# Optimization experiments

Hardware: AMD Instinct MI355X
Metric: run time of the kernel (lower is better)

Reference implementation:

```python
import jax, jax.numpy as jnp
import numpy as np
import math

B, T, D = 2, 2048, 1024
H = 16
DH = D // H  # 64
ROPE_BASE = 10000.0


def _rope_tables(seq_len, d_head, dtype=jnp.float32):
    inv_freq = 1.0 / (ROPE_BASE ** (jnp.arange(0, d_head, 2, dtype=jnp.float32) / d_head))
    pos = jnp.arange(seq_len, dtype=jnp.float32)
    freqs = jnp.outer(pos, inv_freq)            # [T, DH/2]
    emb = jnp.concatenate([freqs, freqs], -1)   # [T, DH]
    return jnp.cos(emb).astype(dtype), jnp.sin(emb).astype(dtype)


def _rotate_half(x):
    half = x.shape[-1] // 2
    return jnp.concatenate([-x[..., half:], x[..., :half]], axis=-1)


def setup_inputs() -> dict:
    key = jax.random.key(0)
    k1, k2, k3 = jax.random.split(key, 3)
    x = jax.random.normal(k1, (B, T, D), dtype=jnp.float32)
    qkv_w = jax.random.normal(k2, (D, 3 * D), dtype=jnp.float32) * (1.0 / math.sqrt(D))
    out_w = jax.random.normal(k3, (D, D), dtype=jnp.float32) * (1.0 / math.sqrt(D))
    out_b = jnp.zeros((D,), dtype=jnp.float32)
    mask = jnp.tril(jnp.ones((T, T), dtype=bool))[None, None]  # causal [1,1,T,T]
    return {"x": x, "mask": mask, "qkv_w": qkv_w, "out_w": out_w, "out_b": out_b}


def reference(x, mask, qkv_w, out_w, out_b):
    Bv, Tv, Dv = x.shape
    qkv = (x @ qkv_w).reshape(Bv, Tv, 3, H, DH)
    # [B, H, T, DH]
    q = jnp.transpose(qkv[:, :, 0], (0, 2, 1, 3))
    k = jnp.transpose(qkv[:, :, 1], (0, 2, 1, 3))
    v = jnp.transpose(qkv[:, :, 2], (0, 2, 1, 3))
    cos, sin = _rope_tables(Tv, DH, x.dtype)
    cos = cos[None, None]  # [1,1,T,DH]
    sin = sin[None, None]
    q = q * cos + _rotate_half(q) * sin
    k = k * cos + _rotate_half(k) * sin
    scores = jnp.einsum('bhqd,bhkd->bhqk', q, k) / math.sqrt(DH)
    scores = jnp.where(mask, scores, -jnp.inf)
    probs = jax.nn.softmax(scores, axis=-1)  # dropout = identity in eval mode
    out = jnp.einsum('bhqk,bhkd->bhqd', probs, v)
    out = jnp.transpose(out, (0, 2, 1, 3)).reshape(Bv, Tv, Dv)
    return out @ out_w + out_b
```

## Files before the change

### kernel.cpp

```cpp
#include <hip/hip_runtime.h>
#include <math.h>

typedef __attribute__((ext_vector_type(8))) short short8;
typedef __attribute__((ext_vector_type(4))) float f32x4;

static __device__ __forceinline__ unsigned short f2bf(float f) {
  unsigned u = __builtin_bit_cast(unsigned, f);
  u += 0x7fffu + ((u >> 16) & 1u);
  return (unsigned short)(u >> 16);
}
static __device__ __forceinline__ float bf2f(unsigned short h) {
  return __builtin_bit_cast(float, ((unsigned)h) << 16);
}
static __device__ __forceinline__ unsigned pack2bf(float a, float b) {
  return (unsigned)f2bf(a) | ((unsigned)f2bf(b) << 16);
}
static __device__ __forceinline__ unsigned pack2bf_t(float a, float b) {
  return __builtin_amdgcn_perm(__builtin_bit_cast(unsigned, b),
                               __builtin_bit_cast(unsigned, a), 0x07060302u);
}

typedef __attribute__((address_space(3))) unsigned short lds_us;
typedef __attribute__((address_space(1))) const unsigned short gbl_us;

static __device__ __forceinline__ void gld_lds16(const unsigned short* g,
                                                 unsigned short* l) {
  __builtin_amdgcn_global_load_lds((gbl_us*)g, (lds_us*)l, 16, 0, 0);
}

__global__ __launch_bounds__(256) void prep(const float* __restrict__ x,
                                            unsigned short* __restrict__ xb,
                                            const float* __restrict__ qkv_w,
                                            unsigned short* __restrict__ wqkvT,
                                            const float* __restrict__ out_w,
                                            unsigned short* __restrict__ woT) {
  __shared__ unsigned short T[64][68];
  const int blk = blockIdx.x;
  if (blk < 2048) {
    int i = (blk * 256 + threadIdx.x) * 8;
    float4 a = *(const float4*)(x + i);
    float4 b = *(const float4*)(x + i + 4);
    ushort4 u0 = {f2bf(a.x), f2bf(a.y), f2bf(a.z), f2bf(a.w)};
    ushort4 u1 = {f2bf(b.x), f2bf(b.y), f2bf(b.z), f2bf(b.w)};
    *(ushort4*)(xb + i) = u0;
    *(ushort4*)(xb + i + 4) = u1;
    return;
  }
  const float* in;
  unsigned short* out;
  int R, C, bx, by;
  if (blk < 2816) {
    in = qkv_w; out = wqkvT; R = 1024; C = 3072;
    bx = (blk - 2048) % 48; by = (blk - 2048) / 48;
  } else {
    in = out_w; out = woT; R = 1024; C = 1024;
    bx = (blk - 2816) % 16; by = (blk - 2816) / 16;
  }
  const int r0 = by * 64, c0 = bx * 64;
  const int tr = threadIdx.x >> 2;
  const int tc = (threadIdx.x & 3) * 16;
#pragma unroll
  for (int j = 0; j < 4; ++j) {
    float4 v = *(const float4*)(in + (size_t)(r0 + tr) * C + c0 + tc + j * 4);
    ushort4 u = {f2bf(v.x), f2bf(v.y), f2bf(v.z), f2bf(v.w)};
    *(ushort4*)&T[tr][tc + j * 4] = u;
  }
  __syncthreads();
  const int oc = tr;
#pragma unroll
  for (int g = 0; g < 4; ++g) {
    ushort4 u;
    u.x = T[tc + g * 4 + 0][oc];
    u.y = T[tc + g * 4 + 1][oc];
    u.z = T[tc + g * 4 + 2][oc];
    u.w = T[tc + g * 4 + 3][oc];
    *(ushort4*)(out + (size_t)(c0 + oc) * R + r0 + tc + g * 4) = u;
  }
}

template <int MODE, int TN>
__global__ __launch_bounds__(256) void gemm_mfma(
    const unsigned short* __restrict__ A, const unsigned short* __restrict__ BT,
    unsigned short* __restrict__ qo, unsigned short* __restrict__ ko,
    unsigned short* __restrict__ vo, const float* __restrict__ bias,
    float* __restrict__ out) {
  constexpr int NTT = TN / 32;
  constexpr int BCH = TN * 4 / 256;
  __shared__ unsigned short As[2][4096];
  __shared__ unsigned short Bs[2][TN * 32];
  const int tid = threadIdx.x;
  const int w = tid >> 6;
  const int lane = tid & 63;
  const int l15 = lane & 15;
  const int quad = lane >> 4;
  const int wm = w >> 1, wn = w & 1;
  const int m0 = blockIdx.y * 128;
  const int n0 = blockIdx.x * TN;

  f32x4 acc[4][NTT];
  const f32x4 zero4 = {0.f, 0.f, 0.f, 0.f};
#pragma unroll
  for (int mt = 0; mt < 4; ++mt)
#pragma unroll
    for (int nt = 0; nt < NTT; ++nt) acc[mt][nt] = zero4;

  int aco[2];
  const unsigned short* gA[2];
#pragma unroll
  for (int i = 0; i < 2; ++i) {
    int c = i * 256 + w * 64 + lane;
    int srow = c >> 2;
    int skch = (c & 3) ^ ((srow >> 1) & 3);
    aco[i] = c * 8;
    gA[i] = A + (size_t)(m0 + srow) * 1024 + skch * 8;
  }
  int bco[BCH];
  const unsigned short* gB[BCH];
#pragma unroll
  for (int i = 0; i < BCH; ++i) {
    int c = i * 256 + w * 64 + lane;
    int srow = c >> 2;
    int skch = (c & 3) ^ ((srow >> 1) & 3);
    bco[i] = c * 8;
    gB[i] = BT + (size_t)(n0 + srow) * 1024 + skch * 8;
  }

  const int swz = (quad ^ ((l15 >> 1) & 3)) * 8;
  int aoff[4], boff[NTT];
#pragma unroll
  for (int t = 0; t < 4; ++t) aoff[t] = (wm * 64 + t * 16 + l15) * 32 + swz;
#pragma unroll
  for (int t = 0; t < NTT; ++t)
    boff[t] = (wn * (TN / 2) + t * 16 + l15) * 32 + swz;

  auto issue = [&](int k0, int buf) {
#pragma unroll
    for (int i = 0; i < 2; ++i) gld_lds16(gA[i] + k0, &As[buf][aco[i]]);
#pragma unroll
    for (int i = 0; i < BCH; ++i) gld_lds16(gB[i] + k0, &Bs[buf][bco[i]]);
  };

  issue(0, 0);
  for (int it = 0; it < 32; ++it) {
    const int cur = it & 1;
    __syncthreads();
    if (it + 1 < 32) issue((it + 1) * 32, cur ^ 1);

    short8 af[4], bf[NTT];
#pragma unroll
    for (int t = 0; t < 4; ++t) af[t] = *(const short8*)(&As[cur][aoff[t]]);
#pragma unroll
    for (int t = 0; t < NTT; ++t) bf[t] = *(const short8*)(&Bs[cur][boff[t]]);
#pragma unroll
    for (int mt = 0; mt < 4; ++mt)
#pragma unroll
      for (int nt = 0; nt < NTT; ++nt)
        acc[mt][nt] =
            __builtin_amdgcn_mfma_f32_16x16x32_bf16(af[mt], bf[nt], acc[mt][nt], 0, 0, 0);
  }

  if constexpr (MODE == 0) {
    const int b = m0 >> 11;
    const int nbase = n0 + wn * 64;
    const int which = nbase >> 10;
    const int h = (nbase & 1023) >> 6;
    const int bh = b * 16 + h;
    if (which < 2) {
      unsigned short* dst = which ? ko : qo;
      const float qs = (which == 0) ? 0.1803368801111f : 1.0f;
      const float INV2PI = 0.15915494309189535f;
      float inv0 = expf(-((float)l15 / 32.f) * 9.21034037198f) * INV2PI;
      float inv1 = expf(-((float)(16 + l15) / 32.f) * 9.21034037198f) * INV2PI;
#pragma unroll
      for (int mt = 0; mt < 4; ++mt)
#pragma unroll
        for (int r = 0; r < 4; ++r) {
          int t = (m0 + wm * 64 + mt * 16 + quad * 4 + r) & 2047;
          float r0 = __builtin_amdgcn_fractf((float)t * inv0);
          float r1 = __builtin_amdgcn_fractf((float)t * inv1);
          float s0 = __builtin_amdgcn_sinf(r0);
          float c0 = __builtin_amdgcn_cosf(r0);
          float s1 = __builtin_amdgcn_sinf(r1);
          float c1 = __builtin_amdgcn_cosf(r1);
          float x0 = acc[mt][0][r], x1 = acc[mt][1][r];
          float x2 = acc[mt][2][r], x3 = acc[mt][3][r];
          size_t rowoff = ((size_t)bh * 2048 + t) * 64 + l15;
          dst[rowoff + 0]  = f2bf((x0 * c0 - x2 * s0) * qs);
          dst[rowoff + 16] = f2bf((x1 * c1 - x3 * s1) * qs);
          dst[rowoff + 32] = f2bf((x2 * c0 + x0 * s0) * qs);
          dst[rowoff + 48] = f2bf((x3 * c1 + x1 * s1) * qs);
        }
    } else {
#pragma unroll
      for (int mt = 0; mt < 4; ++mt) {
        int t0 = (m0 + wm * 64 + mt * 16 + quad * 4) & 2047;
#pragma unroll
        for (int nt = 0; nt < 4; ++nt) {
          int dh = nt * 16 + l15;
          ushort4 st = {f2bf(acc[mt][nt][0]), f2bf(acc[mt][nt][1]),
                        f2bf(acc[mt][nt][2]), f2bf(acc[mt][nt][3])};
          *(ushort4*)(vo + ((size_t)bh * 64 + dh) * 2048 + t0) = st;
        }
      }
    }
  } else {
    const int nbase = n0 + wn * (TN / 2);
    float bv[NTT];
#pragma unroll
    for (int nt = 0; nt < NTT; ++nt) bv[nt] = bias[nbase + nt * 16 + l15];
#pragma unroll
    for (int mt = 0; mt < 4; ++mt)
#pragma unroll
      for (int r = 0; r < 4; ++r) {
        int m = m0 + wm * 64 + mt * 16 + quad * 4 + r;
        float* orow = out + (size_t)m * 1024 + nbase + l15;
#pragma unroll
        for (int nt = 0; nt < NTT; ++nt) orow[nt * 16] = acc[mt][nt][r] + bv[nt];
      }
  }
}

__global__ __launch_bounds__(256) void attn_mfma(
    const unsigned short* __restrict__ qg, const unsigned short* __restrict__ kg,
    const unsigned short* __restrict__ vtg, unsigned short* __restrict__ og,
    unsigned short* __restrict__ OpA,
    unsigned short* __restrict__ OpB,
    float* __restrict__ Lpart) {
  __shared__ unsigned short Ks[2][4096];
  __shared__ unsigned short Vt[2][4096];
  __shared__ unsigned short Ps[4 * 16 * 64];
  const int bh = blockIdx.y;
  const int slot = blockIdx.x;
  int qb, chunk;
  if (slot < 32) {
    qb = 24 + (slot & 7);
    chunk = slot >> 3;
  } else if (slot < 56) {
    int s = slot - 32;
    qb = 16 + (s & 7);
    chunk = s >> 3;
  } else if (slot < 72) {
    int s = slot - 56;
    qb = 8 + (s & 7);
    chunk = s >> 3;
  } else {
    qb = slot - 72;
    chunk = 0;
  }
  const int n = qb >= 24 ? 4 : (qb >= 16 ? 3 : (qb >= 8 ? 2 : 1));
  const int t0 = chunk * (qb + 1) / n;
  const int t1 = (chunk + 1) * (qb + 1) / n;

  const int tid = threadIdx.x;
  const int w = tid >> 6;
  const int lane = tid & 63;
  const int l15 = lane & 15;
  const int quad = lane >> 4;

  const int gq0 = qb * 64;
  const int qw = w * 16;

  const unsigned short* qrow = qg + ((size_t)bh * 2048 + gq0 + qw + l15) * 64;
  short8 qf0 = *(const short8*)(qrow + quad * 8);
  short8 qf1 = *(const short8*)(qrow + quad * 8 + 32);

  f32x4 acc_o[4];
  const f32x4 zero4 = {0.f, 0.f, 0.f, 0.f};
#pragma unroll
  for (int nt = 0; nt < 4; ++nt) acc_o[nt] = zero4;
  f32x4 acc_l = zero4;
  const short one_bf = (short)0x3F80;
  const short8 ones8 = {one_bf, one_bf, one_bf, one_bf,
                        one_bf, one_bf, one_bf, one_bf};

  const unsigned short* kbase = kg + (size_t)bh * 2048 * 64;
  const unsigned short* vtbase = vtg + (size_t)bh * 64 * 2048;
  unsigned short* pb = &Ps[w * 16 * 64];
  const int prow = l15 * 64;
  const int psw = l15 & 7;

  auto issue = [&](int kb, int buf) {
    const unsigned short* ksrc = kbase + (size_t)(kb * 64) * 64;
    const unsigned short* vsrc = vtbase + kb * 64;
#pragma unroll
    for (int i = 0; i < 2; ++i) {
      int c = (w * 2 + i) * 64 + lane;
      int row = c >> 3, d = c & 7;
      int sc = d ^ (row & 7);
      gld_lds16(ksrc + row * 64 + sc * 8, &Ks[buf][c * 8]);
      gld_lds16(vsrc + (size_t)row * 2048 + sc * 8, &Vt[buf][c * 8]);
    }
  };

  const int kc0 = (quad ^ psw) * 8;
  const int kc1 = kc0 ^ 32;

  issue(t0, 0);
  for (int kb = t0; kb < t1; ++kb) {
    const int cur = (kb - t0) & 1;
    __syncthreads();
    if (kb + 1 < t1) issue(kb + 1, cur ^ 1);

    const unsigned short* kt = Ks[cur];
    const unsigned short* vt = Vt[cur];

    f32x4 s[4];
#pragma unroll
    for (int nt = 0; nt < 4; ++nt) {
      const unsigned short* kr = kt + (nt * 16 + l15) * 64;
      short8 kf0 = *(const short8*)(kr + kc0);
      short8 kf1 = *(const short8*)(kr + kc1);
      f32x4 c = zero4;
      c = __builtin_amdgcn_mfma_f32_16x16x32_bf16(kf0, qf0, c, 0, 0, 0);
      c = __builtin_amdgcn_mfma_f32_16x16x32_bf16(kf1, qf1, c, 0, 0, 0);
      s[nt] = c;
    }

    if (kb == qb) {
#pragma unroll
      for (int nt = 0; nt < 4; ++nt) {
        int klocal = nt * 16 + quad * 4;
        int qlocal = qw + l15;
#pragma unroll
        for (int r = 0; r < 4; ++r)
          if (klocal + r > qlocal) s[nt][r] = -INFINITY;
      }
    }

#pragma unroll
    for (int nt = 0; nt < 4; ++nt) {
      float e0 = __builtin_amdgcn_exp2f(s[nt][0]);
      float e1 = __builtin_amdgcn_exp2f(s[nt][1]);
      float e2 = __builtin_amdgcn_exp2f(s[nt][2]);
      float e3 = __builtin_amdgcn_exp2f(s[nt][3]);
      int base = prow + ((nt * 2 + (quad >> 1)) ^ psw) * 8 + (quad & 1) * 4;
      uint2 pk;
      pk.x = pack2bf_t(e0, e1);
      pk.y = pack2bf_t(e2, e3);
      *(uint2*)&pb[base] = pk;
    }

    short8 pf0 = *(const short8*)&pb[prow + (quad ^ psw) * 8];
    short8 pf1 = *(const short8*)&pb[prow + ((4 + quad) ^ psw) * 8];

    acc_l = __builtin_amdgcn_mfma_f32_16x16x32_bf16(ones8, pf0, acc_l, 0, 0, 0);
    acc_l = __builtin_amdgcn_mfma_f32_16x16x32_bf16(ones8, pf1, acc_l, 0, 0, 0);

#pragma unroll
    for (int nt = 0; nt < 4; ++nt) {
      const unsigned short* vr = vt + (nt * 16 + l15) * 64;
      short8 vf0 = *(const short8*)(vr + kc0);
      short8 vf1 = *(const short8*)(vr + kc1);
      acc_o[nt] = __builtin_amdgcn_mfma_f32_16x16x32_bf16(vf0, pf0, acc_o[nt], 0, 0, 0);
      acc_o[nt] = __builtin_amdgcn_mfma_f32_16x16x32_bf16(vf1, pf1, acc_o[nt], 0, 0, 0);
    }
  }

  float lsum = acc_l[0];

  if (n == 1) {
    float inv_l = 1.0f / lsum;
    const int b = bh >> 4;
    const int h = bh & 15;
    unsigned short* orow =
        og + ((size_t)(b * 2048 + gq0 + qw + l15)) * 1024 + h * 64 + quad * 4;
#pragma unroll
    for (int nt = 0; nt < 4; ++nt) {
      *(unsigned*)(orow + nt * 16) =
          pack2bf(acc_o[nt][0] * inv_l, acc_o[nt][1] * inv_l);
      *(unsigned*)(orow + nt * 16 + 2) =
          pack2bf(acc_o[nt][2] * inv_l, acc_o[nt][3] * inv_l);
    }
  } else {
    const int pidx = (qb < 16) ? (qb - 8) * 2 + chunk
                               : (qb < 24) ? 16 + (qb - 16) * 3 + chunk
                                           : 40 + (qb - 24) * 4 + chunk;
    unsigned short* obase = (pidx < 16)
                                ? OpB + ((size_t)(bh * 16 + pidx)) * 4096
                                : OpA + ((size_t)(bh * 56 + (pidx - 16))) * 4096;
    unsigned short* orow = obase + (qw + l15) * 64 + quad * 4;
#pragma unroll
    for (int nt = 0; nt < 4; ++nt) {
      *(unsigned*)(orow + nt * 16) = pack2bf(acc_o[nt][0], acc_o[nt][1]);
      *(unsigned*)(orow + nt * 16 + 2) = pack2bf(acc_o[nt][2], acc_o[nt][3]);
    }
    if (quad == 0) Lpart[(bh * 72 + pidx) * 64 + qw + l15] = lsum;
  }
}

__global__ __launch_bounds__(256) void attn_combine(
    const unsigned short* __restrict__ OpA, const unsigned short* __restrict__ OpB,
    const float* __restrict__ Lpart, unsigned short* __restrict__ og) {
  int i = blockIdx.x * 256 + threadIdx.x;
  int dh = (i & 15) * 4;
  int q = (i >> 4) & 63;
  int idx = i >> 10;
  int bh = idx / 24;
  int qr = idx - bh * 24;
  int qb = 8 + qr;
  int count = qr < 8 ? 2 : (qr < 16 ? 3 : 4);
  int pstart = qr < 8 ? qr * 2 : (qr < 16 ? 16 + (qr - 8) * 3 : 40 + (qr - 16) * 4);
  float o0 = 0.f, o1 = 0.f, o2 = 0.f, o3 = 0.f, l = 0.f;
  for (int c = 0; c < count; ++c) {
    int pidx = pstart + c;
    const unsigned short* obase =
        (pidx < 16) ? OpB + ((size_t)(bh * 16 + pidx)) * 4096
                    : OpA + ((size_t)(bh * 56 + (pidx - 16))) * 4096;
    ushort4 a = *(const ushort4*)(obase + q * 64 + dh);
    o0 += bf2f(a.x);
    o1 += bf2f(a.y);
    o2 += bf2f(a.z);
    o3 += bf2f(a.w);
    l += Lpart[(bh * 72 + pidx) * 64 + q];
  }
  float inv = 1.0f / l;
  int bb = bh >> 4, h = bh & 15;
  int t = qb * 64 + q;
  unsigned short* orow = og + ((size_t)(bb * 2048 + t)) * 1024 + h * 64 + dh;
  *(unsigned*)(orow) = pack2bf(o0 * inv, o1 * inv);
  *(unsigned*)(orow + 2) = pack2bf(o2 * inv, o3 * inv);
}

extern "C" void kernel_launch(void* const* d_in, const int* in_sizes, int n_in,
                              void* d_out, int out_size, void* d_ws,
                              size_t ws_size, hipStream_t stream) {
  const float* x = (const float*)d_in[0];
  const float* qkv_w = (const float*)d_in[2];
  const float* out_w = (const float*)d_in[3];
  const float* out_b = (const float*)d_in[4];
  float* out = (float*)d_out;

  unsigned short* xb = (unsigned short*)d_ws;
  unsigned short* wqkvT = xb + 4194304;
  unsigned short* woT = wqkvT + 3145728;
  unsigned short* qb16 = woT + 1048576;
  unsigned short* kb16 = qb16 + 4194304;
  unsigned short* vt16 = kb16 + 4194304;
  unsigned short* ab = vt16 + 4194304;
  unsigned short* OpB = ab + 4194304;
  float* Lpart = (float*)(OpB + 4194304);
  unsigned short* OpA = xb;

  prep<<<3072, 256, 0, stream>>>(x, xb, qkv_w, wqkvT, out_w, woT);
  gemm_mfma<0, 128><<<dim3(24, 32), 256, 0, stream>>>(
      xb, wqkvT, qb16, kb16, vt16, nullptr, nullptr);
  attn_mfma<<<dim3(80, 32), 256, 0, stream>>>(qb16, kb16, vt16, ab, OpA, OpB,
                                              Lpart);
  attn_combine<<<3072, 256, 0, stream>>>(OpA, OpB, Lpart, ab);
  gemm_mfma<1, 64><<<dim3(16, 32), 256, 0, stream>>>(ab, woT, nullptr, nullptr,
                                                     nullptr, out_b, out);
}
```

Before: 201.2 us.

## Shrink GEMM tiles for more blocks and restructure QKV RoPE epilogue per head

The GEMM kernel is parameterized by TM and TN. The QKV projection now uses 128x64 tiles (48x32 grid) and the output projection uses 64x64 tiles (16x64 grid), which gives more blocks to spread across the CUs. For the QKV mode, each block now covers exactly one head. The B-fragment column mapping is interleaved so that each wave holds paired rotary halves (p and p+32), so every lane computes a single sin/cos pair instead of two. Smaller tiles lower per-block data reuse and increase global and LDS traffic per FLOP.

Result: slower. 215.9 us (+7.3%).

```diff
diff --git a/kernel.cpp b/kernel.cpp
--- a/kernel.cpp
+++ b/kernel.cpp
@@ -78,15 +78,17 @@
   }
 }
 
-template <int MODE, int TN>
+template <int MODE, int TM, int TN>
 __global__ __launch_bounds__(256) void gemm_mfma(
     const unsigned short* __restrict__ A, const unsigned short* __restrict__ BT,
     unsigned short* __restrict__ qo, unsigned short* __restrict__ ko,
     unsigned short* __restrict__ vo, const float* __restrict__ bias,
     float* __restrict__ out) {
+  constexpr int MTT = TM / 32;
   constexpr int NTT = TN / 32;
-  constexpr int BCH = TN * 4 / 256;
-  __shared__ unsigned short As[2][4096];
+  constexpr int ACH = TM / 64;
+  constexpr int BCH = TN / 64;
+  __shared__ unsigned short As[2][TM * 32];
   __shared__ unsigned short Bs[2][TN * 32];
   const int tid = threadIdx.x;
   const int w = tid >> 6;
@@ -94,20 +96,20 @@
   const int l15 = lane & 15;
   const int quad = lane >> 4;
   const int wm = w >> 1, wn = w & 1;
-  const int m0 = blockIdx.y * 128;
+  const int m0 = blockIdx.y * TM;
   const int n0 = blockIdx.x * TN;
 
-  f32x4 acc[4][NTT];
+  f32x4 acc[MTT][NTT];
   const f32x4 zero4 = {0.f, 0.f, 0.f, 0.f};
 #pragma unroll
-  for (int mt = 0; mt < 4; ++mt)
+  for (int mt = 0; mt < MTT; ++mt)
 #pragma unroll
     for (int nt = 0; nt < NTT; ++nt) acc[mt][nt] = zero4;
 
-  int aco[2];
-  const unsigned short* gA[2];
-#pragma unroll
-  for (int i = 0; i < 2; ++i) {
+  int aco[ACH];
+  const unsigned short* gA[ACH];
+#pragma unroll
+  for (int i = 0; i < ACH; ++i) {
     int c = i * 256 + w * 64 + lane;
     int srow = c >> 2;
     int skch = (c & 3) ^ ((srow >> 1) & 3);
@@ -126,16 +128,19 @@
   }
 
   const int swz = (quad ^ ((l15 >> 1) & 3)) * 8;
-  int aoff[4], boff[NTT];
-#pragma unroll
-  for (int t = 0; t < 4; ++t) aoff[t] = (wm * 64 + t * 16 + l15) * 32 + swz;
-#pragma unroll
-  for (int t = 0; t < NTT; ++t)
-    boff[t] = (wn * (TN / 2) + t * 16 + l15) * 32 + swz;
+  int aoff[MTT], boff[NTT];
+#pragma unroll
+  for (int t = 0; t < MTT; ++t)
+    aoff[t] = (wm * (TM / 2) + t * 16 + l15) * 32 + swz;
+#pragma unroll
+  for (int t = 0; t < NTT; ++t) {
+    int colbase = (MODE == 0) ? (wn * 16 + t * 32) : (wn * (TN / 2) + t * 16);
+    boff[t] = (colbase + l15) * 32 + swz;
+  }
 
   auto issue = [&](int k0, int buf) {
 #pragma unroll
-    for (int i = 0; i < 2; ++i) gld_lds16(gA[i] + k0, &As[buf][aco[i]]);
+    for (int i = 0; i < ACH; ++i) gld_lds16(gA[i] + k0, &As[buf][aco[i]]);
 #pragma unroll
     for (int i = 0; i < BCH; ++i) gld_lds16(gB[i] + k0, &Bs[buf][bco[i]]);
   };
@@ -146,13 +151,13 @@
     __syncthreads();
     if (it + 1 < 32) issue((it + 1) * 32, cur ^ 1);
 
-    short8 af[4], bf[NTT];
-#pragma unroll
-    for (int t = 0; t < 4; ++t) af[t] = *(const short8*)(&As[cur][aoff[t]]);
+    short8 af[MTT], bf[NTT];
+#pragma unroll
+    for (int t = 0; t < MTT; ++t) af[t] = *(const short8*)(&As[cur][aoff[t]]);
 #pragma unroll
     for (int t = 0; t < NTT; ++t) bf[t] = *(const short8*)(&Bs[cur][boff[t]]);
 #pragma unroll
-    for (int mt = 0; mt < 4; ++mt)
+    for (int mt = 0; mt < MTT; ++mt)
 #pragma unroll
       for (int nt = 0; nt < NTT; ++nt)
         acc[mt][nt] =
@@ -161,42 +166,35 @@
 
   if constexpr (MODE == 0) {
     const int b = m0 >> 11;
-    const int nbase = n0 + wn * 64;
-    const int which = nbase >> 10;
-    const int h = (nbase & 1023) >> 6;
+    const int which = n0 >> 10;
+    const int h = (n0 & 1023) >> 6;
     const int bh = b * 16 + h;
     if (which < 2) {
       unsigned short* dst = which ? ko : qo;
       const float qs = (which == 0) ? 0.1803368801111f : 1.0f;
-      const float INV2PI = 0.15915494309189535f;
-      float inv0 = expf(-((float)l15 / 32.f) * 9.21034037198f) * INV2PI;
-      float inv1 = expf(-((float)(16 + l15) / 32.f) * 9.21034037198f) * INV2PI;
-#pragma unroll
-      for (int mt = 0; mt < 4; ++mt)
+      const int p = wn * 16 + l15;
+      float inv = __builtin_amdgcn_exp2f((float)p * -0.41524101186f) *
+                  0.15915494309f;
+#pragma unroll
+      for (int mt = 0; mt < MTT; ++mt)
 #pragma unroll
         for (int r = 0; r < 4; ++r) {
-          int t = (m0 + wm * 64 + mt * 16 + quad * 4 + r) & 2047;
-          float r0 = __builtin_amdgcn_fractf((float)t * inv0);
-          float r1 = __builtin_amdgcn_fractf((float)t * inv1);
-          float s0 = __builtin_amdgcn_sinf(r0);
-          float c0 = __builtin_amdgcn_cosf(r0);
-          float s1 = __builtin_amdgcn_sinf(r1);
-          float c1 = __builtin_amdgcn_cosf(r1);
+          int t = (m0 + wm * (TM / 2) + mt * 16 + quad * 4 + r) & 2047;
+          float rv = __builtin_amdgcn_fractf((float)t * inv);
+          float s = __builtin_amdgcn_sinf(rv);
+          float c = __builtin_amdgcn_cosf(rv);
           float x0 = acc[mt][0][r], x1 = acc[mt][1][r];
-          float x2 = acc[mt][2][r], x3 = acc[mt][3][r];
-          size_t rowoff = ((size_t)bh * 2048 + t) * 64 + l15;
-          dst[rowoff + 0]  = f2bf((x0 * c0 - x2 * s0) * qs);
-          dst[rowoff + 16] = f2bf((x1 * c1 - x3 * s1) * qs);
-          dst[rowoff + 32] = f2bf((x2 * c0 + x0 * s0) * qs);
-          dst[rowoff + 48] = f2bf((x3 * c1 + x1 * s1) * qs);
+          size_t rowoff = ((size_t)bh * 2048 + t) * 64;
+          dst[rowoff + p]      = f2bf((x0 * c - x1 * s) * qs);
+          dst[rowoff + p + 32] = f2bf((x1 * c + x0 * s) * qs);
         }
     } else {
 #pragma unroll
-      for (int mt = 0; mt < 4; ++mt) {
-        int t0 = (m0 + wm * 64 + mt * 16 + quad * 4) & 2047;
-#pragma unroll
-        for (int nt = 0; nt < 4; ++nt) {
-          int dh = nt * 16 + l15;
+      for (int mt = 0; mt < MTT; ++mt) {
+        int t0 = (m0 + wm * (TM / 2) + mt * 16 + quad * 4) & 2047;
+#pragma unroll
+        for (int nt = 0; nt < NTT; ++nt) {
+          int dh = wn * 16 + nt * 32 + l15;
           ushort4 st = {f2bf(acc[mt][nt][0]), f2bf(acc[mt][nt][1]),
                         f2bf(acc[mt][nt][2]), f2bf(acc[mt][nt][3])};
           *(ushort4*)(vo + ((size_t)bh * 64 + dh) * 2048 + t0) = st;
@@ -209,10 +207,10 @@
 #pragma unroll
     for (int nt = 0; nt < NTT; ++nt) bv[nt] = bias[nbase + nt * 16 + l15];
 #pragma unroll
-    for (int mt = 0; mt < 4; ++mt)
+    for (int mt = 0; mt < MTT; ++mt)
 #pragma unroll
       for (int r = 0; r < 4; ++r) {
-        int m = m0 + wm * 64 + mt * 16 + quad * 4 + r;
+        int m = m0 + wm * (TM / 2) + mt * 16 + quad * 4 + r;
         float* orow = out + (size_t)m * 1024 + nbase + l15;
 #pragma unroll
         for (int nt = 0; nt < NTT; ++nt) orow[nt * 16] = acc[mt][nt][r] + bv[nt];
@@ -442,11 +440,11 @@
   unsigned short* OpA = xb;
 
   prep<<<3072, 256, 0, stream>>>(x, xb, qkv_w, wqkvT, out_w, woT);
-  gemm_mfma<0, 128><<<dim3(24, 32), 256, 0, stream>>>(
+  gemm_mfma<0, 128, 64><<<dim3(48, 32), 256, 0, stream>>>(
       xb, wqkvT, qb16, kb16, vt16, nullptr, nullptr);
   attn_mfma<<<dim3(80, 32), 256, 0, stream>>>(qb16, kb16, vt16, ab, OpA, OpB,
                                               Lpart);
   attn_combine<<<3072, 256, 0, stream>>>(OpA, OpB, Lpart, ab);
-  gemm_mfma<1, 64><<<dim3(16, 32), 256, 0, stream>>>(ab, woT, nullptr, nullptr,
-                                                     nullptr, out_b, out);
-}
+  gemm_mfma<1, 64, 64><<<dim3(16, 64), 256, 0, stream>>>(
+      ab, woT, nullptr, nullptr, nullptr, out_b, out);
+}
```
